# Performance work log

Measured on AMD Instinct MI355X. Metric: run time of the kernel, lower is better.

Reference implementation:

```python
import jax, jax.numpy as jnp
import numpy as np
import math

SQRT2 = math.sqrt(2.0)


def _rotation_grids(theta_deg, grid_size):
    # torch affine_grid (align_corners=True) base coords for output [G, G]:
    # grid[h, w] = (xs[w], ys[h]) transformed by R = [[c, s, 0], [-s, c, 0]]
    xs = jnp.linspace(-1.0, 1.0, grid_size, dtype=jnp.float32)
    X, Y = jnp.meshgrid(xs, xs)            # [G,G], X varies along width
    th = jnp.deg2rad(theta_deg.astype(jnp.float32))[:, None, None]  # [T,1,1]
    c, s = jnp.cos(th), jnp.sin(th)
    gx = c * X + s * Y                      # [T,G,G]
    gy = -s * X + c * Y
    return gx, gy


def _bilinear_sample(x, gx, gy):
    # x: [N,C,H,W]; gx,gy: [T,G,G] normalized coords in [-1,1]
    # bilinear, zeros padding, align_corners=True -> returns [N,C,T,G,G]
    N, C, H, W = x.shape
    ix = (gx + 1.0) * 0.5 * (W - 1)
    iy = (gy + 1.0) * 0.5 * (H - 1)
    ix0 = jnp.floor(ix)
    iy0 = jnp.floor(iy)
    wx1 = ix - ix0
    wy1 = iy - iy0
    wx0 = 1.0 - wx1
    wy0 = 1.0 - wy1

    def gather(iyf, ixf):
        valid = (ixf >= 0) & (ixf <= W - 1) & (iyf >= 0) & (iyf <= H - 1)
        ii = jnp.clip(ixf, 0, W - 1).astype(jnp.int32)
        jj = jnp.clip(iyf, 0, H - 1).astype(jnp.int32)
        v = x[:, :, jj, ii]                 # [N,C,T,G,G]
        return v * valid.astype(x.dtype)

    return (gather(iy0, ix0) * (wy0 * wx0)
            + gather(iy0, ix0 + 1) * (wy0 * wx1)
            + gather(iy0 + 1, ix0) * (wy1 * wx0)
            + gather(iy0 + 1, ix0 + 1) * (wy1 * wx1))


def radon_forward(x, theta_deg):
    N, C, W, H = x.shape
    # circle=False: pad image to the diagonal size so rotations keep all content
    diagonal = SQRT2 * W
    pad = int(math.ceil(diagonal - W))
    new_center = (W + pad) // 2
    old_center = W // 2
    pad_before = new_center - old_center
    x = jnp.pad(x, ((0, 0), (0, 0), (pad_before, pad - pad_before),
                    (pad_before, pad - pad_before)))
    G = x.shape[-1]                         # padded grid size == ceil(sqrt2*W)
    gx, gy = _rotation_grids(theta_deg, G)  # [T,G,G]
    rotated = _bilinear_sample(x, gx, gy)   # [N,C,T,G,G]
    sino = rotated.sum(axis=3)              # integrate over rows -> [N,C,T,G]
    return jnp.swapaxes(sino, 2, 3)         # [N,C,G,T]


def setup_inputs() -> dict:
    key = jax.random.key(0)
    x = jax.random.normal(key, (2, 1, 256, 256), dtype=jnp.float32)
    theta = jnp.arange(180, dtype=jnp.int64) if jax.config.jax_enable_x64 else jnp.arange(180, dtype=jnp.int32)
    return {"x": x, "theta": theta}


def reference(x, theta):
    return radon_forward(x, theta)
```

## Files before the change

### kernel.cpp

```cpp
#include <hip/hip_runtime.h>
#include <hip/hip_fp16.h>
#include <math.h>


#define G       363
#define NT      180
#define PADB    53
#define STEP    (2.0f / 362.0f)
#define DEG2RAD 0.017453292519943295f

#define TSW     32
#define NJB     12
#define NJBF    6
#define CW      264
#define CH      264

#define GLOAD16(gp, lp) __builtin_amdgcn_global_load_lds(                     \
    (const __attribute__((address_space(1))) void*)(gp),                      \
    (__attribute__((address_space(3))) void*)(lp), 16, 0, 0)

__global__ __launch_bounds__(256) void radon_fwd(
    const float* __restrict__ x, const int* __restrict__ theta,
    float* __restrict__ out)
{
    const int t = blockIdx.x / NJBF, jb = blockIdx.x % NJBF;
    const int jl = threadIdx.x, chunk = threadIdx.y;
    const int j = jb * 64 + jl;
    const float th = (float)theta[t] * DEG2RAD;
    const float c = cosf(th), s = sinf(th);
    const float xj = fmaf((float)j, STEP, -1.0f);
    const float s181 = s * 181.0f, c181 = c * 181.0f;
    const float bx = fmaf(c, xj, 1.0f) * 181.0f;
    const float by = fmaf(-s, xj, 1.0f) * 181.0f;
    const float* img0 = x;
    const float* img1 = x + 65536;
    float acc0 = 0.f, acc1 = 0.f;
    for (int i = chunk; i < G; i += 4) {
        const float xi = fmaf((float)i, STEP, -1.0f);
        const float ix = fmaf(s181, xi, bx);
        const float iy = fmaf(c181, xi, by);
        const float fx = floorf(ix), fy = floorf(iy);
        const int ix0 = (int)fx, iy0 = (int)fy;
        const float wx1 = ix - fx, wy1 = iy - fy;
        const float wx0 = 1.f - wx1, wy0 = 1.f - wy1;
        const int cc0 = ix0 - 53, cc1 = cc0 + 1, rr0 = iy0 - 53, rr1 = rr0 + 1;
        const float wxa = ((unsigned)cc0 < 256u) ? wx0 : 0.f;
        const float wxb = ((unsigned)cc1 < 256u) ? wx1 : 0.f;
        const float wya = ((unsigned)rr0 < 256u) ? wy0 : 0.f;
        const float wyb = ((unsigned)rr1 < 256u) ? wy1 : 0.f;
        const int c0c = min(max(cc0, 0), 255), c1c = min(max(cc1, 0), 255);
        const int r0b = min(max(rr0, 0), 255) << 8, r1b = min(max(rr1, 0), 255) << 8;
        const float w00 = wya * wxa, w01 = wya * wxb, w10 = wyb * wxa, w11 = wyb * wxb;
        acc0 = fmaf(img0[r0b + c0c], w00, acc0);
        acc0 = fmaf(img0[r0b + c1c], w01, acc0);
        acc0 = fmaf(img0[r1b + c0c], w10, acc0);
        acc0 = fmaf(img0[r1b + c1c], w11, acc0);
        acc1 = fmaf(img1[r0b + c0c], w00, acc1);
        acc1 = fmaf(img1[r0b + c1c], w01, acc1);
        acc1 = fmaf(img1[r1b + c0c], w10, acc1);
        acc1 = fmaf(img1[r1b + c1c], w11, acc1);
    }
    __shared__ float red[2][4][64];
    red[0][chunk][jl] = acc0;
    red[1][chunk][jl] = acc1;
    __syncthreads();
    if (threadIdx.y < 2 && j < G) {
        const int n = threadIdx.y;
        out[n * (G * NT) + j * NT + t] =
            red[n][0][jl] + red[n][1][jl] + red[n][2][jl] + red[n][3][jl];
    }
}

__global__ __launch_bounds__(256) void prep_k(
    const float* __restrict__ x,
    unsigned* __restrict__ xIh, unsigned* __restrict__ xTIh)
{
    const int bid = blockIdx.x;
    const int tx = threadIdx.x, ty = threadIdx.y;

    __shared__ unsigned tl[32][33];
    const int cx0 = (bid % 9) * 32, cy0 = (bid / 9) * 32;
    #pragma unroll
    for (int dy = 0; dy < 32; dy += 8) {
        const int cy = cy0 + ty + dy, cx = cx0 + tx;
        const int pr = cy - 4, pc = cx - 4;
        unsigned v = 0u;
        if ((unsigned)pr < 256u && (unsigned)pc < 256u) {
            const int p = pr * 256 + pc;
            const unsigned short a = __half_as_ushort(__float2half_rn(x[p]));
            const unsigned short b = __half_as_ushort(__float2half_rn(x[p + 65536]));
            v = (unsigned)a | ((unsigned)b << 16);
        }
        if (cy < CH && cx < CW) xIh[cy * CW + cx] = v;
        tl[ty + dy][tx] = v;
    }
    __syncthreads();
    #pragma unroll
    for (int dy = 0; dy < 32; dy += 8) {
        const int rp = cx0 + ty + dy, cp = cy0 + tx;
        if (rp < CH && cp < CW) xTIh[rp * CW + cp] = tl[tx][ty + dy];
    }
}

template<bool SAFE>
__device__ __forceinline__ void stage32(char* tileW_b,
    const unsigned* __restrict__ srcC, int r0p, int c0p, int lane)
{
    const int ty0 = lane >> 3;
    const int tx  = (lane & 7) << 2;
    #pragma unroll
    for (int u = 0; u < 4; ++u) {
        const int ty = ty0 + (u << 3);
        int idx;
        if (SAFE) {
            idx = (r0p + 4 + ty) * CW + (c0p + 4 + tx);
        } else {
            const int rc = min(max(r0p + ty, -4), 256) + 4;
            const int cc = min(max(c0p + tx, -4), 256) + 4;
            idx = rc * CW + cc;
        }
        GLOAD16(srcC + idx, tileW_b + (u << 10));
    }
}

template<bool TAIL>
__device__ __forceinline__ void gather6(const unsigned* __restrict__ tl,
    float Uf0, float Vf0, float dU, float dV, int iexc,
    float& a0, float& a1)
{
    __half2 acc = __float2half2_rn(0.0f);
    #pragma unroll
    for (int k = 0; k < 6; ++k) {
        const float Uf = fmaf((float)k, dU, Uf0);
        const float Vf = fmaf((float)k, dV, Vf0);
        const float fU = floorf(Uf), fV = floorf(Vf);
        const float wU1 = Uf - fU;
        const float wV1 = Vf - fV;
        const int rel = (int)fmaf(fU, (float)TSW, fV);
        const __half2 x00 = *(const __half2*)(tl + rel);
        const __half2 x01 = *(const __half2*)(tl + rel + 1);
        const __half2 x10 = *(const __half2*)(tl + rel + TSW);
        const __half2 x11 = *(const __half2*)(tl + rel + TSW + 1);
        const __half2 wv2 = __float2half2_rn(wV1);
        const __half2 wu2 = __float2half2_rn(wU1);
        const __half2 t0 = __hfma2(wv2, __hsub2(x01, x00), x00);
        const __half2 t1 = __hfma2(wv2, __hsub2(x11, x10), x10);
        __half2 v = __hfma2(wu2, __hsub2(t1, t0), t0);
        if (TAIL && k >= iexc) v = __float2half2_rn(0.0f);
        acc = __hadd2(acc, v);
    }
    a0 += __low2float(acc);
    a1 += __high2float(acc);
}

__global__ __launch_bounds__(256) void radon_wv(
    const unsigned* __restrict__ xIh, const unsigned* __restrict__ xTIh,
    const int* __restrict__ theta, float* __restrict__ out)
{
    __shared__ unsigned tile[4 * TSW * TSW];
    __shared__ float red[4][2][16];

    const int blk  = blockIdx.x;
    const int t    = blk / NJB;
    const int jb   = blk - t * NJB;
    const int tid  = threadIdx.x;
    const int lane = tid & 63;
    const int wid  = tid >> 6;
    const int wj   = wid & 1;
    const int wi   = wid >> 1;
    const int jl   = lane & 15;
    const int kk   = lane >> 4;

    unsigned* tileW = tile + wid * (TSW * TSW);
    char*     tileW_b = (char*)tileW;

    const float th = (float)theta[t] * DEG2RAD;
    const float c = cosf(th), s = sinf(th);
    const float s181 = s * 181.0f, c181 = c * 181.0f;

    const int caseA = (fabsf(c) >= fabsf(s));
    const unsigned* __restrict__ srcC = caseA ? xIh : xTIh;

    const float slopeU = caseA ? c181 : s181;
    const float slopeV = caseA ? s181 : c181;
    const float dU = slopeU * STEP;
    const float dV = slopeV * STEP;

    const int   j  = jb * 32 + wj * 16 + jl;
    const float xj = fmaf((float)j, STEP, -1.0f);
    const float bx = fmaf(c,  xj, 1.0f) * 181.0f;
    const float by = fmaf(-s, xj, 1.0f) * 181.0f;
    const float U00L = (caseA ? by : bx) - slopeU;
    const float V00L = (caseA ? bx : by) - slopeV;

    const int   j0  = jb * 32 + wj * 16;
    const float xjm = fmaf((float)j0,        STEP, -1.0f);
    const float xjM = fmaf((float)(j0 + 15), STEP, -1.0f);
    const float bxm = fmaf(c,  xjm, 1.0f) * 181.0f;
    const float bym = fmaf(-s, xjm, 1.0f) * 181.0f;
    const float bxM = fmaf(c,  xjM, 1.0f) * 181.0f;
    const float byM = fmaf(-s, xjM, 1.0f) * 181.0f;
    const float U00m = (caseA ? bym : bxm) - slopeU;
    const float U00M = (caseA ? byM : bxM) - slopeU;
    const float V00m = (caseA ? bxm : bym) - slopeV;
    const float V00M = (caseA ? bxM : byM) - slopeV;

    const float fiofs = (float)(kk * 6);

    float a0 = 0.f, a1 = 0.f;

    for (int sub = 0; sub < 8; ++sub) {
        const int i0 = (wi * 8 + sub) * 24;
        const float fi0 = (float)i0, fi1 = (float)(i0 + 23);

        const float Umin = fminf(fminf(fmaf(dU, fi0, U00m), fmaf(dU, fi0, U00M)),
                                 fminf(fmaf(dU, fi1, U00m), fmaf(dU, fi1, U00M)));
        const float Vmin = fminf(fminf(fmaf(dV, fi0, V00m), fmaf(dV, fi0, V00M)),
                                 fminf(fmaf(dV, fi1, V00m), fmaf(dV, fi1, V00M)));
        const int r0 = __builtin_amdgcn_readfirstlane((int)floorf(Umin) - 1);
        const int c0 = __builtin_amdgcn_readfirstlane((int)floorf(Vmin) - 1);
        const int r0p = r0 - PADB, c0p = c0 - PADB;

        asm volatile("s_waitcnt lgkmcnt(0)" ::: "memory");
        __builtin_amdgcn_sched_barrier(0);

        if (r0p >= -4 && r0p <= 228 && c0p >= -4 && c0p <= 228)
            stage32<true >(tileW_b, srcC, r0p, c0p, lane);
        else
            stage32<false>(tileW_b, srcC, r0p, c0p, lane);

        asm volatile("s_waitcnt vmcnt(0)" ::: "memory");
        __builtin_amdgcn_sched_barrier(0);

        const float fi  = fi0 + fiofs;
        const float Uf0 = fmaf(dU, fi, U00L) - (float)r0;
        const float Vf0 = fmaf(dV, fi, V00L) - (float)c0;
        const int ibase = i0 + kk * 6;

        if (i0 + 23 < G) {
            gather6<false>(tileW, Uf0, Vf0, dU, dV, 6, a0, a1);
        } else {
            gather6<true>(tileW, Uf0, Vf0, dU, dV, G - ibase, a0, a1);
        }
    }

    a0 += __shfl_xor(a0, 16); a1 += __shfl_xor(a1, 16);
    a0 += __shfl_xor(a0, 32); a1 += __shfl_xor(a1, 32);

    if (lane < 16) {
        red[wid][0][lane] = a0;
        red[wid][1][lane] = a1;
    }
    __syncthreads();

    if (tid < 64) {
        const int n = tid >> 5, jj = tid & 31;
        const int wj2 = jj >> 4, jl2 = jj & 15;
        const float v = red[wj2][n][jl2] + red[wj2 + 2][n][jl2];
        const int jo = jb * 32 + jj;
        if (jo < G)
            out[(n * G + jo) * NT + t] = v;
    }
}

extern "C" void kernel_launch(void* const* d_in, const int* in_sizes, int n_in,
                              void* d_out, int out_size, void* d_ws, size_t ws_size,
                              hipStream_t stream) {
    const float* x     = (const float*)d_in[0];
    const int*   theta = (const int*)d_in[1];
    float*       out   = (float*)d_out;

    const size_t XIH_OFF  = 0;
    const size_t XTIH_OFF = (size_t)CH * CW * 4;
    const size_t NEED     = 2 * XTIH_OFF;

    if (ws_size < NEED) {
        hipLaunchKernelGGL(radon_fwd, dim3(NT * NJBF), dim3(64, 4), 0, stream,
                           x, theta, out);
        return;
    }

    unsigned* xIh  = (unsigned*)((char*)d_ws + XIH_OFF);
    unsigned* xTIh = (unsigned*)((char*)d_ws + XTIH_OFF);

    hipLaunchKernelGGL(prep_k, dim3(81), dim3(32, 8), 0, stream,
                       x, xIh, xTIh);
    hipLaunchKernelGGL(radon_wv, dim3(NT * NJB), dim3(256), 0, stream,
                       xIh, xTIh, theta, out);
}
```

Before: 33.19 us.

## Double-buffer per-wave LDS tiles with smaller 24-row stages and prefetch

Each wave now stages a smaller 24x32 tile covering 12 projection rows instead of a 32x32 tile covering 24 rows, and keeps two LDS buffers. The load for the next sub-step is issued before gathering from the current buffer, with a partial vmcnt wait, so global-to-LDS transfers overlap the bilinear gather work. This is meant to hide the exposed load latency of the previous load-then-wait loop. The cost is twice as many sub-iterations, each with its own bounding-box and waitcnt overhead, and a small increase in LDS use.

```diff
diff --git a/kernel.cpp b/kernel.cpp
--- a/kernel.cpp
+++ b/kernel.cpp
@@ -10,6 +10,8 @@
 #define DEG2RAD 0.017453292519943295f
 
 #define TSW     32
+#define TRW     24
+#define TCELLS  (TRW * TSW)
 #define NJB     12
 #define NJBF    6
 #define CW      264
@@ -103,13 +105,13 @@
 }
 
 template<bool SAFE>
-__device__ __forceinline__ void stage32(char* tileW_b,
+__device__ __forceinline__ void stage24(char* buf_b,
     const unsigned* __restrict__ srcC, int r0p, int c0p, int lane)
 {
     const int ty0 = lane >> 3;
     const int tx  = (lane & 7) << 2;
     #pragma unroll
-    for (int u = 0; u < 4; ++u) {
+    for (int u = 0; u < 3; ++u) {
         const int ty = ty0 + (u << 3);
         int idx;
         if (SAFE) {
@@ -119,18 +121,18 @@
             const int cc = min(max(c0p + tx, -4), 256) + 4;
             idx = rc * CW + cc;
         }
-        GLOAD16(srcC + idx, tileW_b + (u << 10));
+        GLOAD16(srcC + idx, buf_b + (u << 10));
     }
 }
 
 template<bool TAIL>
-__device__ __forceinline__ void gather6(const unsigned* __restrict__ tl,
+__device__ __forceinline__ void gather3(const unsigned* __restrict__ tl,
     float Uf0, float Vf0, float dU, float dV, int iexc,
     float& a0, float& a1)
 {
     __half2 acc = __float2half2_rn(0.0f);
     #pragma unroll
-    for (int k = 0; k < 6; ++k) {
+    for (int k = 0; k < 3; ++k) {
         const float Uf = fmaf((float)k, dU, Uf0);
         const float Vf = fmaf((float)k, dV, Vf0);
         const float fU = floorf(Uf), fV = floorf(Vf);
@@ -153,11 +155,11 @@
     a1 += __high2float(acc);
 }
 
-__global__ __launch_bounds__(256) void radon_wv(
+__global__ __launch_bounds__(256) void radon_wv2(
     const unsigned* __restrict__ xIh, const unsigned* __restrict__ xTIh,
     const int* __restrict__ theta, float* __restrict__ out)
 {
-    __shared__ unsigned tile[4 * TSW * TSW];
+    __shared__ unsigned tile[4 * 2 * TCELLS];
     __shared__ float red[4][2][16];
 
     const int blk  = blockIdx.x;
@@ -171,8 +173,7 @@
     const int jl   = lane & 15;
     const int kk   = lane >> 4;
 
-    unsigned* tileW = tile + wid * (TSW * TSW);
-    char*     tileW_b = (char*)tileW;
+    unsigned* tileW = tile + wid * (2 * TCELLS);
 
     const float th = (float)theta[t] * DEG2RAD;
     const float c = cosf(th), s = sinf(th);
@@ -205,43 +206,63 @@
     const float V00m = (caseA ? bxm : bym) - slopeV;
     const float V00M = (caseA ? bxM : byM) - slopeV;
 
-    const float fiofs = (float)(kk * 6);
-
-    float a0 = 0.f, a1 = 0.f;
-
-    for (int sub = 0; sub < 8; ++sub) {
-        const int i0 = (wi * 8 + sub) * 24;
-        const float fi0 = (float)i0, fi1 = (float)(i0 + 23);
-
+    const float fiofs = (float)(kk * 3);
+    const int   nsub  = wi ? 15 : 16;
+    const int   isub0 = wi * 16;
+
+    auto bboxmins = [&](int sub, int& r0o, int& c0o) {
+        const int i0 = (isub0 + sub) * 12;
+        const float fi0 = (float)i0, fi1 = (float)(i0 + 11);
         const float Umin = fminf(fminf(fmaf(dU, fi0, U00m), fmaf(dU, fi0, U00M)),
                                  fminf(fmaf(dU, fi1, U00m), fmaf(dU, fi1, U00M)));
         const float Vmin = fminf(fminf(fmaf(dV, fi0, V00m), fmaf(dV, fi0, V00M)),
                                  fminf(fmaf(dV, fi1, V00m), fmaf(dV, fi1, V00M)));
-        const int r0 = __builtin_amdgcn_readfirstlane((int)floorf(Umin) - 1);
-        const int c0 = __builtin_amdgcn_readfirstlane((int)floorf(Vmin) - 1);
+        r0o = __builtin_amdgcn_readfirstlane((int)floorf(Umin) - 1);
+        c0o = __builtin_amdgcn_readfirstlane((int)floorf(Vmin) - 1);
+    };
+    auto dostage = [&](int bufsel, int r0, int c0) {
+        char* b = (char*)(tileW + bufsel * TCELLS);
         const int r0p = r0 - PADB, c0p = c0 - PADB;
-
-        asm volatile("s_waitcnt lgkmcnt(0)" ::: "memory");
+        if (r0p >= -4 && r0p <= 236 && c0p >= -4 && c0p <= 228)
+            stage24<true >(b, srcC, r0p, c0p, lane);
+        else
+            stage24<false>(b, srcC, r0p, c0p, lane);
+    };
+
+    float a0 = 0.f, a1 = 0.f;
+
+    int r0c, c0c;
+    bboxmins(0, r0c, c0c);
+    dostage(0, r0c, c0c);
+
+    for (int sub = 0; sub < nsub; ++sub) {
+        int r0n = 0, c0n = 0;
+        const bool pf = (sub + 1) < nsub;
+        if (pf) {
+            bboxmins(sub + 1, r0n, c0n);
+            asm volatile("s_waitcnt lgkmcnt(0)" ::: "memory");
+            __builtin_amdgcn_sched_barrier(0);
+            dostage((sub + 1) & 1, r0n, c0n);
+            asm volatile("s_waitcnt vmcnt(3)" ::: "memory");
+        } else {
+            asm volatile("s_waitcnt vmcnt(0)" ::: "memory");
+        }
         __builtin_amdgcn_sched_barrier(0);
 
-        if (r0p >= -4 && r0p <= 228 && c0p >= -4 && c0p <= 228)
-            stage32<true >(tileW_b, srcC, r0p, c0p, lane);
-        else
-            stage32<false>(tileW_b, srcC, r0p, c0p, lane);
-
-        asm volatile("s_waitcnt vmcnt(0)" ::: "memory");
-        __builtin_amdgcn_sched_barrier(0);
-
-        const float fi  = fi0 + fiofs;
-        const float Uf0 = fmaf(dU, fi, U00L) - (float)r0;
-        const float Vf0 = fmaf(dV, fi, V00L) - (float)c0;
-        const int ibase = i0 + kk * 6;
-
-        if (i0 + 23 < G) {
-            gather6<false>(tileW, Uf0, Vf0, dU, dV, 6, a0, a1);
+        const unsigned* buf = tileW + (sub & 1) * TCELLS;
+        const int i0 = (isub0 + sub) * 12;
+        const float fi  = (float)i0 + fiofs;
+        const float Uf0 = fmaf(dU, fi, U00L) - (float)r0c;
+        const float Vf0 = fmaf(dV, fi, V00L) - (float)c0c;
+        const int ibase = i0 + kk * 3;
+
+        if (i0 + 11 < G) {
+            gather3<false>(buf, Uf0, Vf0, dU, dV, 3, a0, a1);
         } else {
-            gather6<true>(tileW, Uf0, Vf0, dU, dV, G - ibase, a0, a1);
+            gather3<true>(buf, Uf0, Vf0, dU, dV, G - ibase, a0, a1);
         }
+
+        r0c = r0n; c0c = c0n;
     }
 
     a0 += __shfl_xor(a0, 16); a1 += __shfl_xor(a1, 16);
@@ -285,6 +306,6 @@
 
     hipLaunchKernelGGL(prep_k, dim3(81), dim3(32, 8), 0, stream,
                        x, xIh, xTIh);
-    hipLaunchKernelGGL(radon_wv, dim3(NT * NJB), dim3(256), 0, stream,
+    hipLaunchKernelGGL(radon_wv2, dim3(NT * NJB), dim3(256), 0, stream,
                        xIh, xTIh, theta, out);
 }
```

After: 39.98 us. 1.2x slower.
